# Kernel optimization log

Hardware: AMD Instinct MI355X
Metric: run time of the kernel (lower is better)

The kernel has to match this reference:

```python
import jax, jax.numpy as jnp
import numpy as np

N, E = 50000, 800000
IN, HID, OUT = 256, 128, 128


def setup_inputs() -> dict:
    key = jax.random.key(0)
    ks = jax.random.split(key, 6)
    x = jax.random.normal(ks[0], (N, IN), dtype=jnp.float32)
    edge_index = jax.random.randint(ks[1], (2, E), 0, N, dtype=jnp.int32)
    # xavier_normal-ish scales (exact init values irrelevant for correctness baseline)
    W1 = jax.random.normal(ks[2], (IN, HID), dtype=jnp.float32) * (1.414 / np.sqrt(IN))
    att_src = jax.random.normal(ks[3], (HID,), dtype=jnp.float32) * 0.1
    att_dst = jax.random.normal(ks[4], (HID,), dtype=jnp.float32) * 0.1
    W2 = jax.random.normal(ks[5], (HID, OUT), dtype=jnp.float32) * (1.414 / np.sqrt(HID))
    return {"x": x, "edge_index": edge_index, "W1": W1,
            "att_src": att_src, "att_dst": att_dst, "W2": W2}


def _gat_layer(x, edge_index, W, a_src, a_dst):
    """GATConv(heads=1, concat=False, add_self_loops=False, dropout=0), attention=True."""
    n = x.shape[0]
    src, dst = edge_index[0], edge_index[1]  # message x_j = h[src], grouped by index = dst
    h = x @ W                                 # (N, C)
    e_src = h @ a_src                         # (N,) per-node attention logits
    e_dst = h @ a_dst                         # (N,)
    # per-edge: sigmoid(alpha_j + alpha_i), then scatter-softmax over dst neighborhoods
    alpha = jax.nn.sigmoid(e_src[src] + e_dst[dst])             # (E,)
    m = jax.ops.segment_max(alpha, dst, num_segments=n)          # stable softmax max
    ex = jnp.exp(alpha - m[dst])
    denom = jax.ops.segment_sum(ex, dst, num_segments=n)
    w = ex / denom[dst]                                          # (E,)
    # scatter-add aggregation of weighted source features; heads=1 so mean over heads is identity
    return jax.ops.segment_sum(h[src] * w[:, None], dst, num_segments=n)  # (N, C)


def reference(x, edge_index, W1, att_src, att_dst, W2):
    h1 = jax.nn.elu(_gat_layer(x, edge_index, W1, att_src, att_dst))
    # conv2 called with attention=False: mm(h1, W2).view(N,1,C).mean(1) == plain linear
    return h1 @ W2
```

## Files before the change

kernel.cpp:

```cpp
#include <hip/hip_runtime.h>
#include <hip/hip_bf16.h>

#define N_NODES 50000
#define N_EDGES 800000
#define DIN 256
#define DHID 128
#define DOUT 128
#define NBUCK 196
#define BINBLK 256
#define EPB 3125
#define G1TILES 391

typedef __attribute__((ext_vector_type(8))) short bf16x8;
typedef __attribute__((ext_vector_type(4))) float f32x4;

__device__ inline unsigned short f2b(float f) {
    __hip_bfloat16 b = __float2bfloat16(f);
    return *reinterpret_cast<unsigned short*>(&b);
}

__global__ __launch_bounds__(1024) void convW_lhist_kernel(
    const float* __restrict__ W1, const float* __restrict__ W2,
    const int* __restrict__ ei,
    unsigned short* __restrict__ W1t, unsigned short* __restrict__ W2t,
    int* __restrict__ blockHistT)
{
    __shared__ int h[NBUCK];
    const int blk = blockIdx.x;
    const int tid = threadIdx.x;

    if (blk < 48) {
        int i = blk * 1024 + tid;
        if (i < DIN * DHID) {
            int n = i >> 8, k = i & 255;
            int kt = k >> 5, q = (k >> 3) & 3, e = k & 7;
            int t = n >> 4, m = n & 15;
            W1t[(((kt * 8 + t) * 64) + (q * 16 + m)) * 8 + e] = f2b(W1[k * DHID + n]);
        } else {
            int j = i - DIN * DHID;
            int n = j >> 7, k = j & 127;
            int kt = k >> 5, q = (k >> 3) & 3, e = k & 7;
            int t = n >> 4, m = n & 15;
            W2t[(((kt * 8 + t) * 64) + (q * 16 + m)) * 8 + e] = f2b(W2[k * DOUT + n]);
        }
        return;
    }

    const int b = blk - 48;
    if (tid < NBUCK) h[tid] = 0;
    __syncthreads();
    const int base = b * EPB;
    #pragma unroll 1
    for (int it = 0; it < 4; ++it) {
        int e = base + it * 1024 + tid;
        if (e < base + EPB)
            atomicAdd(&h[ei[N_EDGES + e] >> 8], 1);
    }
    __syncthreads();
    if (tid < 256) blockHistT[b * 256 + tid] = (tid < NBUCK) ? h[tid] : 0;
}

__global__ __launch_bounds__(256) void gemm1_scan_kernel(
    const float* __restrict__ x,
    const unsigned short* __restrict__ W1t,
    const float* __restrict__ att_src,
    const float* __restrict__ att_dst,
    const int* __restrict__ blockHistT,
    unsigned short* __restrict__ hb,
    float* __restrict__ es,
    float* __restrict__ ed,
    int* __restrict__ matrixScan)
{
    __shared__ int bs[256];
    __shared__ int sc[256];
    const int tid = threadIdx.x;

    if (blockIdx.x >= G1TILES) {
        const int b = blockIdx.x - G1TILES;

        int tot = 0;
        #pragma unroll 4
        for (int p = 0; p < 256; ++p) tot += blockHistT[p * 256 + tid];
        bs[tid] = tot;
        __syncthreads();
        #pragma unroll
        for (int off = 1; off < 256; off <<= 1) {
            int u = (tid >= off) ? bs[tid - off] : 0;
            __syncthreads();
            bs[tid] += u;
            __syncthreads();
        }
        const int base = (b == 0) ? 0 : bs[b - 1];

        int c = blockHistT[tid * 256 + b];
        sc[tid] = c;
        __syncthreads();
        #pragma unroll
        for (int off = 1; off < 256; off <<= 1) {
            int u = (tid >= off) ? sc[tid - off] : 0;
            __syncthreads();
            sc[tid] += u;
            __syncthreads();
        }
        matrixScan[b * 256 + tid] = base + sc[tid] - c;
        return;
    }

    const int wave = tid >> 6, lane = tid & 63;
    const int row0 = blockIdx.x * 128 + wave * 32;
    const int m = lane & 15, q = lane >> 4;

    int r0 = row0 + m;
    int r1 = row0 + 16 + m;
    int rc0 = (r0 < N_NODES) ? r0 : 0;
    int rc1 = (r1 < N_NODES) ? r1 : 0;

    f32x4 acc0[8], acc1[8];
    #pragma unroll
    for (int t = 0; t < 8; ++t) {
        acc0[t] = (f32x4){0.f, 0.f, 0.f, 0.f};
        acc1[t] = (f32x4){0.f, 0.f, 0.f, 0.f};
    }

    const float* xr0 = x + (size_t)rc0 * DIN + q * 8;
    const float* xr1 = x + (size_t)rc1 * DIN + q * 8;
    const short* wb  = (const short*)W1t + lane * 8;

    #pragma unroll
    for (int kt = 0; kt < 8; ++kt) {
        float4 f0 = *(const float4*)(xr0 + kt * 32);
        float4 f1 = *(const float4*)(xr0 + kt * 32 + 4);
        float4 g0 = *(const float4*)(xr1 + kt * 32);
        float4 g1 = *(const float4*)(xr1 + kt * 32 + 4);
        bf16x8 a0, a1;
        a0[0] = (short)f2b(f0.x); a0[1] = (short)f2b(f0.y);
        a0[2] = (short)f2b(f0.z); a0[3] = (short)f2b(f0.w);
        a0[4] = (short)f2b(f1.x); a0[5] = (short)f2b(f1.y);
        a0[6] = (short)f2b(f1.z); a0[7] = (short)f2b(f1.w);
        a1[0] = (short)f2b(g0.x); a1[1] = (short)f2b(g0.y);
        a1[2] = (short)f2b(g0.z); a1[3] = (short)f2b(g0.w);
        a1[4] = (short)f2b(g1.x); a1[5] = (short)f2b(g1.y);
        a1[6] = (short)f2b(g1.z); a1[7] = (short)f2b(g1.w);
        #pragma unroll
        for (int t = 0; t < 8; ++t) {
            bf16x8 b = *(const bf16x8*)(wb + (kt * 8 + t) * 512);
            acc0[t] = __builtin_amdgcn_mfma_f32_16x16x32_bf16(a0, b, acc0[t], 0, 0, 0);
            acc1[t] = __builtin_amdgcn_mfma_f32_16x16x32_bf16(a1, b, acc1[t], 0, 0, 0);
        }
    }

    #pragma unroll
    for (int reg = 0; reg < 4; ++reg) {
        int ra = row0 + q * 4 + reg;
        int rb = row0 + 16 + q * 4 + reg;
        if (ra < N_NODES) {
            #pragma unroll
            for (int t = 0; t < 8; ++t)
                hb[(size_t)ra * DHID + t * 16 + m] = f2b(acc0[t][reg]);
        }
        if (rb < N_NODES) {
            #pragma unroll
            for (int t = 0; t < 8; ++t)
                hb[(size_t)rb * DHID + t * 16 + m] = f2b(acc1[t][reg]);
        }
    }

    float es0[4] = {0,0,0,0}, ed0[4] = {0,0,0,0};
    float es1[4] = {0,0,0,0}, ed1[4] = {0,0,0,0};
    #pragma unroll
    for (int t = 0; t < 8; ++t) {
        float as = att_src[t * 16 + m];
        float ad = att_dst[t * 16 + m];
        #pragma unroll
        for (int reg = 0; reg < 4; ++reg) {
            es0[reg] += acc0[t][reg] * as;
            ed0[reg] += acc0[t][reg] * ad;
            es1[reg] += acc1[t][reg] * as;
            ed1[reg] += acc1[t][reg] * ad;
        }
    }
    #pragma unroll
    for (int off = 8; off; off >>= 1)
        #pragma unroll
        for (int reg = 0; reg < 4; ++reg) {
            es0[reg] += __shfl_xor(es0[reg], off);
            ed0[reg] += __shfl_xor(ed0[reg], off);
            es1[reg] += __shfl_xor(es1[reg], off);
            ed1[reg] += __shfl_xor(ed1[reg], off);
        }
    if (m == 0) {
        #pragma unroll
        for (int reg = 0; reg < 4; ++reg) {
            int ra = row0 + q * 4 + reg;
            int rb = row0 + 16 + q * 4 + reg;
            if (ra < N_NODES) { es[ra] = es0[reg]; ed[ra] = ed0[reg]; }
            if (rb < N_NODES) { es[rb] = es1[reg]; ed[rb] = ed1[reg]; }
        }
    }
}

__global__ __launch_bounds__(1024) void binpass_kernel(
    const int* __restrict__ ei,
    const float* __restrict__ es,
    const float* __restrict__ ed,
    const int* __restrict__ matrixScan,
    int2* __restrict__ binned)
{
    __shared__ int lcur[NBUCK];
    const int t = threadIdx.x, blk = blockIdx.x;
    if (t < NBUCK) lcur[t] = matrixScan[t * 256 + blk];
    __syncthreads();
    const int base = blk * EPB;
    #pragma unroll 1
    for (int it = 0; it < 4; ++it) {
        int e = base + it * 1024 + t;
        if (e < base + EPB) {
            int s = ei[e];
            int d = ei[N_EDGES + e];
            float a  = es[s] + ed[d];
            float sg = 1.f / (1.f + __expf(-a));
            float w  = __expf(sg);
            int pos = atomicAdd(&lcur[d >> 8], 1);
            binned[pos] = make_int2(s | ((d & 255) << 16), __float_as_int(w));
        }
    }
}

__global__ __launch_bounds__(1024) void sortpass_kernel(
    const int2* __restrict__ binned,
    const int* __restrict__ matrixScan,
    int2* __restrict__ sortedSW,
    int* __restrict__ offset,
    int* __restrict__ count)
{
    __shared__ int lhist[256], lscan[256], lcur[256];
    const int t = threadIdx.x, b = blockIdx.x;
    const int start = matrixScan[b * 256];
    const int end   = (b == NBUCK - 1) ? N_EDGES : matrixScan[(b + 1) * 256];
    const int cnt   = end - start;

    if (t < 256) lhist[t] = 0;
    __syncthreads();
    for (int i = t; i < cnt; i += 1024)
        atomicAdd(&lhist[(binned[start + i].x >> 16) & 255], 1);
    __syncthreads();

    int v = 0;
    if (t < 256) { v = lhist[t]; lscan[t] = v; }
    __syncthreads();
    #pragma unroll
    for (int off = 1; off < 256; off <<= 1) {
        int u = 0;
        if (t < 256 && t >= off) u = lscan[t - off];
        __syncthreads();
        if (t < 256) lscan[t] += u;
        __syncthreads();
    }
    if (t < 256) {
        int excl = lscan[t] - v;
        int node = (b << 8) + t;
        if (node < N_NODES) { offset[node] = start + excl; count[node] = v; }
        lcur[t] = excl;
    }
    __syncthreads();

    for (int i = t; i < cnt; i += 1024) {
        int2 ent = binned[start + i];
        int dlow = (ent.x >> 16) & 255;
        int pos = atomicAdd(&lcur[dlow], 1);
        sortedSW[start + pos] = make_int2(ent.x & 0xFFFF, ent.y);
    }
}

__global__ __launch_bounds__(256) void agg_kernel(
    const int2* __restrict__ sortedSW,
    const int* __restrict__ offset,
    const int* __restrict__ count,
    const unsigned short* __restrict__ hb,
    unsigned int* __restrict__ h1b)
{
    int node = (blockIdx.x * 256 + threadIdx.x) >> 6;
    int lane = threadIdx.x & 63;
    if (node >= N_NODES) return;

    int beg = offset[node];
    int deg = count[node];

    float2 acc = make_float2(0.f, 0.f);
    float wsum = 0.f;

    for (int base = 0; base < deg; base += 64) {
        int cnt = min(64, deg - base);
        int2 sw = (lane < cnt) ? sortedSW[beg + base + lane] : make_int2(0, 0);
        int j = 0;

#define TIER(T)                                                                 \
        for (; j + T <= cnt; j += T) {                                          \
            unsigned uu[T]; float ww[T];                                        \
            _Pragma("unroll")                                                   \
            for (int k = 0; k < T; ++k) {                                       \
                int s_ = __builtin_amdgcn_readlane(sw.x, j + k);                \
                uu[k] = *(const unsigned*)(hb + (size_t)s_ * DHID + 2 * lane);  \
            }                                                                   \
            _Pragma("unroll")                                                   \
            for (int k = 0; k < T; ++k)                                         \
                ww[k] = __uint_as_float(                                        \
                    (unsigned)__builtin_amdgcn_readlane(sw.y, j + k));          \
            _Pragma("unroll")                                                   \
            for (int k = 0; k < T; ++k) {                                       \
                wsum  += ww[k];                                                 \
                acc.x += ww[k] * __uint_as_float(uu[k] << 16);                  \
                acc.y += ww[k] * __uint_as_float(uu[k] & 0xffff0000u);          \
            }                                                                   \
        }

        TIER(8)
        TIER(4)
#undef TIER
        for (; j < cnt; ++j) {
            int   sj = __builtin_amdgcn_readlane(sw.x, j);
            float wj = __uint_as_float((unsigned)__builtin_amdgcn_readlane(sw.y, j));
            unsigned u = *(const unsigned*)(hb + (size_t)sj * DHID + 2 * lane);
            acc.x += wj * __uint_as_float(u << 16);
            acc.y += wj * __uint_as_float(u & 0xffff0000u);
            wsum  += wj;
        }
    }
    float inv = (deg > 0) ? 1.f / wsum : 0.f;
    float v0 = acc.x * inv, v1 = acc.y * inv;
    float e0 = v0 > 0.f ? v0 : (__expf(v0) - 1.f);
    float e1 = v1 > 0.f ? v1 : (__expf(v1) - 1.f);
    h1b[(size_t)node * (DHID / 2) + lane] =
        (unsigned)f2b(e0) | ((unsigned)f2b(e1) << 16);
}

__global__ __launch_bounds__(256) void gemm2_mfma(
    const unsigned short* __restrict__ h1b,
    const unsigned short* __restrict__ W2t,
    float* __restrict__ out)
{
    const int tid = threadIdx.x;
    const int wave = tid >> 6, lane = tid & 63;
    const int row0 = blockIdx.x * 128 + wave * 32;
    const int m = lane & 15, q = lane >> 4;

    int r0 = row0 + m;
    int r1 = row0 + 16 + m;
    int rc0 = (r0 < N_NODES) ? r0 : 0;
    int rc1 = (r1 < N_NODES) ? r1 : 0;

    f32x4 acc0[8], acc1[8];
    #pragma unroll
    for (int t = 0; t < 8; ++t) {
        acc0[t] = (f32x4){0.f, 0.f, 0.f, 0.f};
        acc1[t] = (f32x4){0.f, 0.f, 0.f, 0.f};
    }

    const short* xp0 = (const short*)h1b + (size_t)rc0 * DHID + q * 8;
    const short* xp1 = (const short*)h1b + (size_t)rc1 * DHID + q * 8;
    const short* wb  = (const short*)W2t + lane * 8;

    #pragma unroll
    for (int kt = 0; kt < 4; ++kt) {
        bf16x8 a0 = *(const bf16x8*)(xp0 + kt * 32);
        bf16x8 a1 = *(const bf16x8*)(xp1 + kt * 32);
        #pragma unroll
        for (int t = 0; t < 8; ++t) {
            bf16x8 b = *(const bf16x8*)(wb + (kt * 8 + t) * 512);
            acc0[t] = __builtin_amdgcn_mfma_f32_16x16x32_bf16(a0, b, acc0[t], 0, 0, 0);
            acc1[t] = __builtin_amdgcn_mfma_f32_16x16x32_bf16(a1, b, acc1[t], 0, 0, 0);
        }
    }

    #pragma unroll
    for (int reg = 0; reg < 4; ++reg) {
        int ra = row0 + q * 4 + reg;
        int rb = row0 + 16 + q * 4 + reg;
        if (ra < N_NODES) {
            #pragma unroll
            for (int t = 0; t < 8; ++t)
                out[(size_t)ra * DOUT + t * 16 + m] = acc0[t][reg];
        }
        if (rb < N_NODES) {
            #pragma unroll
            for (int t = 0; t < 8; ++t)
                out[(size_t)rb * DOUT + t * 16 + m] = acc1[t][reg];
        }
    }
}

extern "C" void kernel_launch(void* const* d_in, const int* in_sizes, int n_in,
                              void* d_out, int out_size, void* d_ws, size_t ws_size,
                              hipStream_t stream)
{
    const float* x    = (const float*)d_in[0];
    const int*   ei   = (const int*)d_in[1];
    const float* W1   = (const float*)d_in[2];
    const float* asrc = (const float*)d_in[3];
    const float* adst = (const float*)d_in[4];
    const float* W2   = (const float*)d_in[5];
    float*       out  = (float*)d_out;

    char* p = (char*)d_ws;
    unsigned short* hb  = (unsigned short*)p;  p += (size_t)N_NODES * DHID * 2;
    unsigned int*   h1b = (unsigned int*)p;    p += (size_t)N_NODES * DHID * 2;
    unsigned short* W1t = (unsigned short*)p;  p += (size_t)DHID * DIN * 2;
    unsigned short* W2t = (unsigned short*)p;  p += (size_t)DOUT * DHID * 2;
    float* es     = (float*)p;  p += (size_t)N_NODES * 4;
    float* ed     = (float*)p;  p += (size_t)N_NODES * 4;
    int*   offset = (int*)p;    p += (size_t)N_NODES * 4;
    int*   count  = (int*)p;    p += (size_t)N_NODES * 4;
    int*   blockHistT   = (int*)p; p += (size_t)256 * 256 * 4;
    int*   matrixScan   = (int*)p; p += (size_t)NBUCK * 256 * 4;
    int2*  binned   = (int2*)p; p += (size_t)N_EDGES * 8;
    int2*  sortedSW = (int2*)p; p += (size_t)N_EDGES * 8;

    convW_lhist_kernel<<<48 + BINBLK, 1024, 0, stream>>>(W1, W2, ei, W1t, W2t, blockHistT);

    gemm1_scan_kernel<<<G1TILES + NBUCK, 256, 0, stream>>>(
        x, W1t, asrc, adst, blockHistT, hb, es, ed, matrixScan);

    binpass_kernel  <<<BINBLK, 1024, 0, stream>>>(ei, es, ed, matrixScan, binned);
    sortpass_kernel <<<NBUCK, 1024, 0, stream>>>(binned, matrixScan, sortedSW, offset, count);
    agg_kernel<<<(N_NODES * 64 + 255) / 256, 256, 0, stream>>>(
        sortedSW, offset, count, hb, h1b);
    gemm2_mfma<<<G1TILES, 256, 0, stream>>>((const unsigned short*)h1b, W2t, out);
}
```

Measured before the change: 181.8 us.

## Fuse neighbor aggregation with second-layer GEMM via shared-memory tile

```diff
diff --git a/kernel.cpp b/kernel.cpp
--- a/kernel.cpp
+++ b/kernel.cpp
@@ -10,6 +10,7 @@
 #define BINBLK 256
 #define EPB 3125
 #define G1TILES 391
+#define HTP 136
 
 typedef __attribute__((ext_vector_type(8))) short bf16x8;
 typedef __attribute__((ext_vector_type(4))) float f32x4;
@@ -272,120 +273,99 @@
     }
 }
 
-__global__ __launch_bounds__(256) void agg_kernel(
+__global__ __launch_bounds__(256) void aggemm2_kernel(
     const int2* __restrict__ sortedSW,
     const int* __restrict__ offset,
     const int* __restrict__ count,
     const unsigned short* __restrict__ hb,
-    unsigned int* __restrict__ h1b)
-{
-    int node = (blockIdx.x * 256 + threadIdx.x) >> 6;
-    int lane = threadIdx.x & 63;
-    if (node >= N_NODES) return;
-
-    int beg = offset[node];
-    int deg = count[node];
-
-    float2 acc = make_float2(0.f, 0.f);
-    float wsum = 0.f;
-
-    for (int base = 0; base < deg; base += 64) {
-        int cnt = min(64, deg - base);
-        int2 sw = (lane < cnt) ? sortedSW[beg + base + lane] : make_int2(0, 0);
-        int j = 0;
-
-#define TIER(T)                                                                 \
-        for (; j + T <= cnt; j += T) {                                          \
-            unsigned uu[T]; float ww[T];                                        \
-            _Pragma("unroll")                                                   \
-            for (int k = 0; k < T; ++k) {                                       \
-                int s_ = __builtin_amdgcn_readlane(sw.x, j + k);                \
-                uu[k] = *(const unsigned*)(hb + (size_t)s_ * DHID + 2 * lane);  \
-            }                                                                   \
-            _Pragma("unroll")                                                   \
-            for (int k = 0; k < T; ++k)                                         \
-                ww[k] = __uint_as_float(                                        \
-                    (unsigned)__builtin_amdgcn_readlane(sw.y, j + k));          \
-            _Pragma("unroll")                                                   \
-            for (int k = 0; k < T; ++k) {                                       \
-                wsum  += ww[k];                                                 \
-                acc.x += ww[k] * __uint_as_float(uu[k] << 16);                  \
-                acc.y += ww[k] * __uint_as_float(uu[k] & 0xffff0000u);          \
-            }                                                                   \
-        }
-
-        TIER(8)
-        TIER(4)
-#undef TIER
-        for (; j < cnt; ++j) {
-            int   sj = __builtin_amdgcn_readlane(sw.x, j);
-            float wj = __uint_as_float((unsigned)__builtin_amdgcn_readlane(sw.y, j));
-            unsigned u = *(const unsigned*)(hb + (size_t)sj * DHID + 2 * lane);
-            acc.x += wj * __uint_as_float(u << 16);
-            acc.y += wj * __uint_as_float(u & 0xffff0000u);
-            wsum  += wj;
-        }
-    }
-    float inv = (deg > 0) ? 1.f / wsum : 0.f;
-    float v0 = acc.x * inv, v1 = acc.y * inv;
-    float e0 = v0 > 0.f ? v0 : (__expf(v0) - 1.f);
-    float e1 = v1 > 0.f ? v1 : (__expf(v1) - 1.f);
-    h1b[(size_t)node * (DHID / 2) + lane] =
-        (unsigned)f2b(e0) | ((unsigned)f2b(e1) << 16);
-}
-
-__global__ __launch_bounds__(256) void gemm2_mfma(
-    const unsigned short* __restrict__ h1b,
     const unsigned short* __restrict__ W2t,
     float* __restrict__ out)
 {
+    __shared__ unsigned short ht[16][HTP];
     const int tid = threadIdx.x;
-    const int wave = tid >> 6, lane = tid & 63;
-    const int row0 = blockIdx.x * 128 + wave * 32;
+    const int wv = tid >> 6, lane = tid & 63;
+    const int nbase = blockIdx.x * 16;
+
+    #pragma unroll 1
+    for (int s = 0; s < 4; ++s) {
+        const int row = wv * 4 + s;
+        const int node = nbase + row;
+
+        int beg = offset[node];
+        int deg = count[node];
+
+        float2 acc = make_float2(0.f, 0.f);
+        float wsum = 0.f;
+
+        for (int bb = 0; bb < deg; bb += 64) {
+            int cnt = min(64, deg - bb);
+            int2 sw = (lane < cnt) ? sortedSW[beg + bb + lane] : make_int2(0, 0);
+            int j = 0;
+
+#define TIER(T)                                                                 \
+            for (; j + T <= cnt; j += T) {                                      \
+                unsigned uu[T]; float ww[T];                                    \
+                _Pragma("unroll")                                               \
+                for (int k = 0; k < T; ++k) {                                   \
+                    int s_ = __builtin_amdgcn_readlane(sw.x, j + k);            \
+                    uu[k] = *(const unsigned*)(hb + (size_t)s_ * DHID + 2 * lane);\
+                }                                                               \
+                _Pragma("unroll")                                               \
+                for (int k = 0; k < T; ++k)                                     \
+                    ww[k] = __uint_as_float(                                    \
+                        (unsigned)__builtin_amdgcn_readlane(sw.y, j + k));      \
+                _Pragma("unroll")                                               \
+                for (int k = 0; k < T; ++k) {                                   \
+                    wsum  += ww[k];                                             \
+                    acc.x += ww[k] * __uint_as_float(uu[k] << 16);              \
+                    acc.y += ww[k] * __uint_as_float(uu[k] & 0xffff0000u);      \
+                }                                                               \
+            }
+
+            TIER(16)
+            TIER(8)
+            TIER(4)
+#undef TIER
+            for (; j < cnt; ++j) {
+                int   sj = __builtin_amdgcn_readlane(sw.x, j);
+                float wj = __uint_as_float((unsigned)__builtin_amdgcn_readlane(sw.y, j));
+                unsigned u = *(const unsigned*)(hb + (size_t)sj * DHID + 2 * lane);
+                acc.x += wj * __uint_as_float(u << 16);
+                acc.y += wj * __uint_as_float(u & 0xffff0000u);
+                wsum  += wj;
+            }
+        }
+        float inv = (deg > 0) ? 1.f / wsum : 0.f;
+        float v0 = acc.x * inv, v1 = acc.y * inv;
+        float e0 = v0 > 0.f ? v0 : (__expf(v0) - 1.f);
+        float e1 = v1 > 0.f ? v1 : (__expf(v1) - 1.f);
+        *(unsigned*)&ht[row][2 * lane] =
+            (unsigned)f2b(e0) | ((unsigned)f2b(e1) << 16);
+    }
+    __syncthreads();
+
     const int m = lane & 15, q = lane >> 4;
 
-    int r0 = row0 + m;
-    int r1 = row0 + 16 + m;
-    int rc0 = (r0 < N_NODES) ? r0 : 0;
-    int rc1 = (r1 < N_NODES) ? r1 : 0;
-
-    f32x4 acc0[8], acc1[8];
-    #pragma unroll
-    for (int t = 0; t < 8; ++t) {
-        acc0[t] = (f32x4){0.f, 0.f, 0.f, 0.f};
-        acc1[t] = (f32x4){0.f, 0.f, 0.f, 0.f};
-    }
-
-    const short* xp0 = (const short*)h1b + (size_t)rc0 * DHID + q * 8;
-    const short* xp1 = (const short*)h1b + (size_t)rc1 * DHID + q * 8;
-    const short* wb  = (const short*)W2t + lane * 8;
+    f32x4 c0 = (f32x4){0.f, 0.f, 0.f, 0.f};
+    f32x4 c1 = (f32x4){0.f, 0.f, 0.f, 0.f};
+
+    const short* wb = (const short*)W2t + lane * 8;
+    const int t0 = wv * 2, t1 = wv * 2 + 1;
 
     #pragma unroll
     for (int kt = 0; kt < 4; ++kt) {
-        bf16x8 a0 = *(const bf16x8*)(xp0 + kt * 32);
-        bf16x8 a1 = *(const bf16x8*)(xp1 + kt * 32);
-        #pragma unroll
-        for (int t = 0; t < 8; ++t) {
-            bf16x8 b = *(const bf16x8*)(wb + (kt * 8 + t) * 512);
-            acc0[t] = __builtin_amdgcn_mfma_f32_16x16x32_bf16(a0, b, acc0[t], 0, 0, 0);
-            acc1[t] = __builtin_amdgcn_mfma_f32_16x16x32_bf16(a1, b, acc1[t], 0, 0, 0);
-        }
+        bf16x8 a = *(const bf16x8*)&ht[m][q * 8 + kt * 32];
+        bf16x8 b0 = *(const bf16x8*)(wb + (kt * 8 + t0) * 512);
+        bf16x8 b1 = *(const bf16x8*)(wb + (kt * 8 + t1) * 512);
+        c0 = __builtin_amdgcn_mfma_f32_16x16x32_bf16(a, b0, c0, 0, 0, 0);
+        c1 = __builtin_amdgcn_mfma_f32_16x16x32_bf16(a, b1, c1, 0, 0, 0);
     }
 
     #pragma unroll
     for (int reg = 0; reg < 4; ++reg) {
-        int ra = row0 + q * 4 + reg;
-        int rb = row0 + 16 + q * 4 + reg;
-        if (ra < N_NODES) {
-            #pragma unroll
-            for (int t = 0; t < 8; ++t)
-                out[(size_t)ra * DOUT + t * 16 + m] = acc0[t][reg];
-        }
-        if (rb < N_NODES) {
-            #pragma unroll
-            for (int t = 0; t < 8; ++t)
-                out[(size_t)rb * DOUT + t * 16 + m] = acc1[t][reg];
-        }
+        int node = nbase + q * 4 + reg;
+        out[(size_t)node * DOUT + t0 * 16 + m] = c0[reg];
+        out[(size_t)node * DOUT + t1 * 16 + m] = c1[reg];
     }
 }
 
@@ -403,7 +383,6 @@
 
     char* p = (char*)d_ws;
     unsigned short* hb  = (unsigned short*)p;  p += (size_t)N_NODES * DHID * 2;
-    unsigned int*   h1b = (unsigned int*)p;    p += (size_t)N_NODES * DHID * 2;
     unsigned short* W1t = (unsigned short*)p;  p += (size_t)DHID * DIN * 2;
     unsigned short* W2t = (unsigned short*)p;  p += (size_t)DOUT * DHID * 2;
     float* es     = (float*)p;  p += (size_t)N_NODES * 4;
@@ -420,9 +399,10 @@
     gemm1_scan_kernel<<<G1TILES + NBUCK, 256, 0, stream>>>(
         x, W1t, asrc, adst, blockHistT, hb, es, ed, matrixScan);
 
-    binpass_kernel  <<<BINBLK, 1024, 0, stream>>>(ei, es, ed, matrixScan, binned);
-    sortpass_kernel <<<NBUCK, 1024, 0, stream>>>(binned, matrixScan, sortedSW, offset, count);
-    agg_kernel<<<(N_NODES * 64 + 255) / 256, 256, 0, stream>>>(
-        sortedSW, offset, count, hb, h1b);
-    gemm2_mfma<<<G1TILES, 256, 0, stream>>>((const unsigned short*)h1b, W2t, out);
-}
+    binpass_kernel<<<BINBLK, 1024, 0, stream>>>(ei, es, ed, matrixScan, binned);
+
+    sortpass_kernel<<<NBUCK, 1024, 0, stream>>>(binned, matrixScan, sortedSW, offset, count);
+
+    aggemm2_kernel<<<(N_NODES + 15) / 16, 256, 0, stream>>>(
+        sortedSW, offset, count, hb, W2t, out);
+}
```

Result: no change. 183.9 us (+1.1%).
